# Kernel optimization log

Measured on AMD Instinct MI355X. Metric: run time of the kernel, lower is better.

## Reference

```python
import jax, jax.numpy as jnp
import numpy as np

B, L, DM = 2, 4096, 1024
DI = 2048      # expand * d_model
DT = 64        # dt_rank = ceil(d_model/16)
K = 4          # d_conv


def _silu(v):
    return v * jax.nn.sigmoid(v)


def setup_inputs() -> dict:
    key = jax.random.key(0)
    ks = jax.random.split(key, 9)
    s = lambda k, shape, sc: jax.random.normal(k, shape, dtype=jnp.float32) * sc
    return {
        "x": s(ks[0], (B, L, DM), 1.0),
        "in_proj_w": s(ks[1], (2 * DI, DM), 0.02),
        "conv_w": s(ks[2], (DI, 1, K), 0.1),   # depthwise: [out=DI, in/groups=1, k]
        "conv_b": s(ks[3], (DI,), 0.02),
        "x_proj_w": s(ks[4], (DT, DI), 0.02),
        "dt_proj_w": s(ks[5], (DI, DT), 0.02),
        "dt_proj_b": s(ks[6], (DI,), 0.02),
        "A_log": jax.random.uniform(ks[7], (DI,), jnp.float32, -3.0, -1.0),
        "D": jnp.ones((DI,), jnp.float32),
        "out_proj_w": s(ks[8], (DM, DI), 0.02),
    }


def reference(x, in_proj_w, conv_w, conv_b, x_proj_w, dt_proj_w, dt_proj_b,
              A_log, D, out_proj_w):
    b, l, _ = x.shape
    # input projection and gate split
    xz = jnp.einsum('bld,ed->ble', x, in_proj_w)          # [b,l,2*DI]
    xi, z = jnp.split(xz, 2, axis=-1)                     # each [b,l,DI]
    # depthwise causal conv1d (torch: padding=K-1 both sides, keep first L)
    xc = jnp.transpose(xi, (0, 2, 1))                     # [b,DI,l]
    xc = jax.lax.conv_general_dilated(
        xc, conv_w, window_strides=(1,), padding=[(K - 1, 0)],
        dimension_numbers=('NCH', 'OIH', 'NCH'),
        feature_group_count=xc.shape[1])
    xc = xc + conv_b[None, :, None]
    xi = _silu(jnp.transpose(xc, (0, 2, 1)))              # [b,l,DI]
    # dt path: x_proj -> dt_rank, dt_proj -> d_inner, softplus + clamp
    dt_low = jnp.einsum('bld,rd->blr', xi, x_proj_w)      # [b,l,DT]
    delta = jax.nn.softplus(jnp.einsum('blr,dr->bld', dt_low, dt_proj_w) + dt_proj_b)
    delta = jnp.clip(delta, 1e-6, 10.0)                   # [b,l,DI]
    A = jnp.clip(-jnp.exp(A_log), -10.0, -1e-6)           # [DI]
    e = jnp.clip(jnp.exp(delta * A), 1e-6, 1.0)           # decay factors [b,l,DI]

    # selective scan: state = clip(state*e + u)
    def step(state, eu):
        et, ut = eu
        state = jnp.clip(state * et + ut, -1e4, 1e4)
        return state, state

    init = jnp.zeros((b, xi.shape[-1]), xi.dtype)
    _, states = jax.lax.scan(step, init,
                             (jnp.swapaxes(e, 0, 1), jnp.swapaxes(xi, 0, 1)))
    y = jnp.swapaxes(states, 0, 1) + xi * D               # skip connection
    y = jnp.clip(y, -1e4, 1e4)
    y = y * _silu(z)                                      # gate
    return jnp.einsum('bld,ed->ble', y, out_proj_w)       # [b,l,DM]
```

## Files before the change

kernel.cpp:

```cpp
#include <hip/hip_runtime.h>
#include <cstdint>
#include <cstddef>

#define B_   2
#define L_   4096
#define DM_  1024
#define DI_  2048
#define DT_  64
#define M_   (B_*L_)
#define G_   64
#define CH_  (L_/G_)
#define KSPL 8
#define KSL  (DI_/KSPL)
#define BK_  32
#define LDC  136
#define LDCF 68
#define LDC3 132

typedef __bf16 bf16;
typedef __bf16 bf16x8 __attribute__((ext_vector_type(8)));
typedef __bf16 bf16x4 __attribute__((ext_vector_type(4)));
typedef float  f32x4  __attribute__((ext_vector_type(4)));

__device__ __forceinline__ float silu_f(float x){ return x / (1.f + __expf(-x)); }
__device__ __forceinline__ float softplus_f(float x){
  return fmaxf(x, 0.f) + __logf(1.f + __expf(-fabsf(x)));
}
__device__ __forceinline__ float e_of(float delta, float Ad){
  float ee = __expf(delta * Ad);
  return fminf(fmaxf(ee, 1e-6f), 1.f);
}
__device__ __forceinline__ float a_of(const float* alog, int d){
  float Ad = -__expf(alog[d]);
  return fminf(fmaxf(Ad, -10.f), -1e-6f);
}

__device__ __forceinline__ void gl_lds16(const bf16* g, bf16* l){
  __builtin_amdgcn_global_load_lds(
      (const __attribute__((address_space(1))) void*)g,
      (__attribute__((address_space(3))) void*)l, 16, 0, 0);
}

__global__ __launch_bounds__(256)
void cvt_all_kernel(const float4* __restrict__ s0, bf16x4* __restrict__ d0, int n0,
                    const float4* __restrict__ s1, bf16x4* __restrict__ d1, int n1,
                    const float4* __restrict__ s2, bf16x4* __restrict__ d2, int n2,
                    const float4* __restrict__ s3, bf16x4* __restrict__ d3, int n3,
                    const float4* __restrict__ s4, bf16x4* __restrict__ d4, int n4)
{
  int i = blockIdx.x*256 + threadIdx.x;
  const float4* s; bf16x4* d;
  if      (i < n0)                 { s = s0; d = d0; }
  else if ((i -= n0) < n1)         { s = s1; d = d1; }
  else if ((i -= n1) < n2)         { s = s2; d = d2; }
  else if ((i -= n2) < n3)         { s = s3; d = d3; }
  else if ((i -= n3) < n4)         { s = s4; d = d4; }
  else return;
  float4 v = s[i];
  bf16x4 o = {(bf16)v.x, (bf16)v.y, (bf16)v.z, (bf16)v.w};
  d[i] = o;
}

template<int EPI, int MT, int NT, int KT>
__global__ __launch_bounds__(256)
void gemm_bt(const bf16* __restrict__ A, const bf16* __restrict__ W,
             float* __restrict__ o0, bf16* __restrict__ ob, bf16* __restrict__ ob2,
             const float* __restrict__ bias, const float* __restrict__ alog,
             const bf16* __restrict__ uq, float* __restrict__ Pq,
             float* __restrict__ Fq)
{
  __shared__ char smem[34816];
  bf16* As = (bf16*)smem;
  bf16* Bs = (bf16*)(smem + 128*BK_*2);
  const int t    = threadIdx.x;
  const int lane = t & 63;
  const int wave = t >> 6;
  const int wm   = wave >> 1, wn = wave & 1;
  const int l16  = lane & 15, quad = lane >> 4;

  int m0, n0;
  if (EPI == 4){
    m0 = blockIdx.y * 128; n0 = 0;
  } else {
    const int gx  = NT / 128;
    const int lin = blockIdx.y * gx + blockIdx.x;
    const int grp = lin / (gx * 4);
    const int rem = lin % (gx * 4);
    m0 = (grp * 4 + (rem & 3)) * 128;
    n0 = (rem >> 2) * 128;
  }

  const int srow = (lane >> 2);
  const int scol = (lane & 3) * 8;

  const int KFULL = (EPI == 4) ? (KT * KSPL) : KT;
  const int kbase = (EPI == 4) ? (int)blockIdx.z * KT : 0;

  const int rowA0 = m0 + wave*32 + srow;
  int rB0 = n0 + wave*32 + srow, rB1 = rB0 + 16;
  if (NT < 128){ rB0 = (rB0 >= NT) ? NT-1 : rB0; rB1 = (rB1 >= NT) ? NT-1 : rB1; }
  const bf16* ap0 = A + (size_t)rowA0*KFULL        + kbase + scol;
  const bf16* ap1 = A + (size_t)(rowA0+16)*KFULL   + kbase + scol;
  const bf16* bp0 = W + (size_t)rB0*KFULL          + kbase + scol;
  const bf16* bp1 = W + (size_t)rB1*KFULL          + kbase + scol;
  bf16* lA0 = &As[(wave*32)*BK_];
  bf16* lA1 = &As[(wave*32+16)*BK_];
  bf16* lB0 = &Bs[(wave*32)*BK_];
  bf16* lB1 = &Bs[(wave*32+16)*BK_];

  f32x4 acc[4][4] = {};
  constexpr int kframes = KT / BK_;

  for (int kt = 0; kt < kframes; ++kt){
    gl_lds16(ap0, lA0);  gl_lds16(ap1, lA1);
    gl_lds16(bp0, lB0);  gl_lds16(bp1, lB1);
    ap0 += BK_; ap1 += BK_; bp0 += BK_; bp1 += BK_;
    __syncthreads();
    bf16x8 af[4], bf_[4];
    #pragma unroll
    for (int i = 0; i < 4; ++i){
      af[i]  = *(const bf16x8*)&As[(wm*64 + i*16 + l16)*BK_ + quad*8];
      bf_[i] = *(const bf16x8*)&Bs[(wn*64 + i*16 + l16)*BK_ + quad*8];
    }
    #pragma unroll
    for (int mi = 0; mi < 4; ++mi)
      #pragma unroll
      for (int ni = 0; ni < 4; ++ni)
        acc[mi][ni] = __builtin_amdgcn_mfma_f32_16x16x32_bf16(af[mi], bf_[ni], acc[mi][ni], 0, 0, 0);
    __syncthreads();
  }

  if (EPI == 3){
    float* Cf = (float*)smem;
    #pragma unroll
    for (int pass = 0; pass < 2; ++pass){
      if (wm == pass){
        #pragma unroll
        for (int mi = 0; mi < 4; ++mi)
          #pragma unroll
          for (int ni = 0; ni < 4; ++ni)
            #pragma unroll
            for (int r = 0; r < 4; ++r)
              Cf[(mi*16 + quad*4 + r)*LDC3 + wn*64 + ni*16 + l16] = acc[mi][ni][r];
      }
      __syncthreads();
      #pragma unroll
      for (int it = 0; it < 8; ++it){
        const int row = it*8 + (t >> 5);
        const int c4  = (t & 31) * 4;
        float4 v = *(const float4*)&Cf[row*LDC3 + c4];
        *(float4*)&o0[(size_t)(m0 + pass*64 + row)*NT + n0 + c4] = v;
      }
      __syncthreads();
    }
  } else if (EPI == 4){
    float* Cf = (float*)smem;
    if (wn == 0){
      #pragma unroll
      for (int mi = 0; mi < 4; ++mi)
        #pragma unroll
        for (int ni = 0; ni < 4; ++ni)
          #pragma unroll
          for (int r = 0; r < 4; ++r)
            Cf[(wm*64 + mi*16 + quad*4 + r)*LDCF + ni*16 + l16] = acc[mi][ni][r];
    }
    __syncthreads();
    #pragma unroll
    for (int it = 0; it < 8; ++it){
      const int row = it*16 + (t >> 4);
      const int c4  = (t & 15) * 4;
      float4 v = *(const float4*)&Cf[row*LDCF + c4];
      *(float4*)&o0[((size_t)blockIdx.z*M_ + m0 + row)*DT_ + c4] = v;
    }
  } else {
    bf16* Cs = (bf16*)smem;
    #pragma unroll
    for (int mi = 0; mi < 4; ++mi){
      #pragma unroll
      for (int ni = 0; ni < 4; ++ni){
        const int n = n0 + wn*64 + ni*16 + l16;
        #pragma unroll
        for (int r = 0; r < 4; ++r){
          float v = acc[mi][ni][r];
          if (EPI == 0){
            if (n0 >= DI_) v = silu_f(v);
          } else {
            v = softplus_f(v + bias[n]);
            v = fminf(fmaxf(v, 1e-6f), 10.f);
          }
          Cs[(wm*64 + mi*16 + quad*4 + r)*LDC + wn*64 + ni*16 + l16] = (bf16)v;
        }
      }
    }
    __syncthreads();
    #pragma unroll
    for (int it = 0; it < 8; ++it){
      const int row = it*16 + (t >> 4);
      const int c8  = (t & 15) * 8;
      bf16x8 v = *(const bf16x8*)&Cs[row*LDC + c8];
      if (EPI == 0){
        if (n0 < DI_) *(bf16x8*)&ob [(size_t)(m0+row)*DI_ + n0        + c8] = v;
        else          *(bf16x8*)&ob2[(size_t)(m0+row)*DI_ + n0 - DI_  + c8] = v;
      } else {
        *(bf16x8*)&ob[(size_t)(m0+row)*NT + n0 + c8] = v;
      }
    }
    if (EPI == 2){
      const int chunk = t >> 7;
      const int dcol  = t & 127;
      const int dglob = n0 + dcol;
      const float Ad  = a_of(alog, dglob);
      const int b  = m0 >> 12;
      const int c0 = (m0 & 4095) >> 6;
      const size_t ubase = (size_t)(m0 + chunk*64)*DI_ + dglob;
      float p = 1.f, f = 0.f;
      for (int i = 0; i < CH_; ++i){
        float dl = (float)Cs[(chunk*64 + i)*LDC + dcol];
        float ee = e_of(dl, Ad);
        float uu = (float)uq[ubase + (size_t)i*DI_];
        f = f*ee + uu;
        p *= ee;
      }
      const size_t o = ((size_t)(b*G_ + c0 + chunk))*DI_ + dglob;
      Pq[o] = p; Fq[o] = f;
    }
  }
}

__global__ __launch_bounds__(256)
void dt_reduce_kernel(const float* __restrict__ part, bf16* __restrict__ dtl){
  const int i = blockIdx.x*256 + threadIdx.x;
  float s = 0.f;
  #pragma unroll
  for (int z = 0; z < KSPL; ++z) s += part[(size_t)z*M_*DT_ + i];
  dtl[i] = (bf16)s;
}

__global__ __launch_bounds__(256)
void conv_silu_kernel(const bf16* __restrict__ xi, const float* __restrict__ cw,
                      const float* __restrict__ cb, bf16* __restrict__ ubf)
{
  const int idx = blockIdx.x*256 + threadIdx.x;
  const int d = idx & (DI_-1);
  const int l = (idx >> 11) & (L_-1);
  float s = cb[d];
  #pragma unroll
  for (int k = 0; k < 4; ++k){
    const int ll = l + k - 3;
    if (ll >= 0) s += (float)xi[idx + (k-3)*DI_] * cw[d*4 + k];
  }
  ubf[idx] = (bf16)silu_f(s);
}

__global__ __launch_bounds__(256)
void scan_pass3(const bf16* __restrict__ delta, const bf16* __restrict__ u,
                const bf16* __restrict__ g, const float* __restrict__ P,
                const float* __restrict__ F, const float* __restrict__ alog,
                const float* __restrict__ Dp, bf16* __restrict__ y)
{
  const int d = blockIdx.x*256 + threadIdx.x;
  const int c = blockIdx.y, b = blockIdx.z;
  const float Ad = a_of(alog, d);
  float s = 0.f;
  for (int cc = 0; cc < c; ++cc){
    const size_t o = ((size_t)(b*G_ + cc))*DI_ + d;
    s = F[o] + P[o]*s;
  }
  size_t base = ((size_t)(b*L_ + c*CH_))*DI_ + d;
  const float Dd = Dp[d];
  for (int i = 0; i < CH_; ++i){
    const size_t idx = base + (size_t)i*DI_;
    const float uu = (float)u[idx];
    s = s*e_of((float)delta[idx], Ad) + uu;
    float yy = s + uu*Dd;
    yy = fminf(fmaxf(yy, -1e4f), 1e4f);
    yy *= (float)g[idx];
    y[idx] = (bf16)yy;
  }
}

extern "C" void kernel_launch(void* const* d_in, const int* in_sizes, int n_in,
                              void* d_out, int out_size, void* d_ws, size_t ws_size,
                              hipStream_t stream)
{
  (void)in_sizes; (void)n_in; (void)out_size; (void)ws_size;
  const float* x        = (const float*)d_in[0];
  const float* in_w     = (const float*)d_in[1];
  const float* conv_w   = (const float*)d_in[2];
  const float* conv_b   = (const float*)d_in[3];
  const float* xproj_w  = (const float*)d_in[4];
  const float* dtproj_w = (const float*)d_in[5];
  const float* dtproj_b = (const float*)d_in[6];
  const float* A_log    = (const float*)d_in[7];
  const float* Dp       = (const float*)d_in[8];
  const float* out_w    = (const float*)d_in[9];

  char* base = (char*)d_ws;
  const size_t MiB = 1024*1024;
  bf16*  xi_bf = (bf16*) (base + 0);
  float* part  = (float*)(base + 0);
  bf16*  dl_bf = (bf16*) (base + 0);
  bf16*  x_bf  = (bf16*) (base + 32*MiB);
  bf16*  w1_bf = (bf16*) (base + 48*MiB);
  bf16*  g_bf  = (bf16*) (base + 64*MiB);
  bf16*  u_bf  = (bf16*) (base + 96*MiB);
  bf16*  y_bf  = (bf16*) (base + 128*MiB);
  bf16*  wo_bf = (bf16*) (base + 160*MiB);
  bf16*  xp_bf = (bf16*) (base + 164*MiB);
  bf16*  dp_bf = (bf16*) (base + 165*MiB);
  bf16*  dtl_bf= (bf16*) (base + 166*MiB);
  float* P     = (float*)(base + 167*MiB);
  float* F     = (float*)(base + 168*MiB);

  const int c0 = (M_*DM_)/4, c1 = (2*DI_*DM_)/4, c2 = (DT_*DI_)/4,
            c3 = (DI_*DT_)/4, c4 = (DM_*DI_)/4;
  const int ctot = c0+c1+c2+c3+c4;
  cvt_all_kernel<<<(ctot+255)/256, 256, 0, stream>>>(
      (const float4*)x,        (bf16x4*)x_bf,  c0,
      (const float4*)in_w,     (bf16x4*)w1_bf, c1,
      (const float4*)xproj_w,  (bf16x4*)xp_bf, c2,
      (const float4*)dtproj_w, (bf16x4*)dp_bf, c3,
      (const float4*)out_w,    (bf16x4*)wo_bf, c4);

  gemm_bt<0, M_, 2*DI_, DM_><<<dim3((2*DI_)/128, M_/128), 256, 0, stream>>>(
      x_bf, w1_bf, nullptr, xi_bf, g_bf, nullptr,
      nullptr, nullptr, nullptr, nullptr);
  conv_silu_kernel<<<(M_*DI_)/256, 256, 0, stream>>>(xi_bf, conv_w, conv_b, u_bf);
  gemm_bt<4, M_, DT_, KSL><<<dim3(1, M_/128, KSPL), 256, 0, stream>>>(
      u_bf, xp_bf, part, nullptr, nullptr, nullptr,
      nullptr, nullptr, nullptr, nullptr);
  dt_reduce_kernel<<<(M_*DT_)/256, 256, 0, stream>>>(part, dtl_bf);
  gemm_bt<2, M_, DI_, DT_><<<dim3(DI_/128, M_/128), 256, 0, stream>>>(
      dtl_bf, dp_bf, nullptr, dl_bf, nullptr, dtproj_b,
      A_log, u_bf, P, F);
  scan_pass3<<<dim3(DI_/256, G_, B_), 256, 0, stream>>>(
      dl_bf, u_bf, g_bf, P, F, A_log, Dp, y_bf);
  gemm_bt<3, M_, DM_, DI_><<<dim3(DM_/128, M_/128), 256, 0, stream>>>(
      y_bf, wo_bf, (float*)d_out, nullptr, nullptr, nullptr,
      nullptr, nullptr, nullptr, nullptr);
}
```

Before: 419.7 us.

## Replace in_proj GEMM with 256x256-tile double-buffered direct-to-LDS kernel

Adds a dedicated gemm256 kernel for the input projection. It uses 512 threads and 256x256 output tiles, loads global memory directly into swizzled LDS with double buffering, and remaps blocks so that groups of them share tiles. Wave priority is raised around the MFMA bursts. The aim is more data reuse per tile and better overlap of loads with compute than the generic 128x128 gemm_bt. The cost is 128KB of LDS per block, which limits occupancy, and a more complex epilogue that writes the output in two passes.

After: 405.2 us. 3.5% less time.

```diff
diff --git a/kernel.cpp b/kernel.cpp
--- a/kernel.cpp
+++ b/kernel.cpp
@@ -61,6 +61,135 @@
   d[i] = o;
 }
 
+template<int MT, int NT, int KT>
+__global__ __launch_bounds__(512, 2)
+void gemm256(const bf16* __restrict__ A, const bf16* __restrict__ W,
+             bf16* __restrict__ ob, bf16* __restrict__ ob2)
+{
+  __shared__ __align__(16) char smem[131072];
+  char* lA = smem;
+  char* lB = smem + 65536;
+
+  const int t    = threadIdx.x;
+  const int lane = t & 63;
+  const int wave = t >> 6;
+  const int wm   = wave >> 2;
+  const int wn   = wave & 3;
+  const int l16  = lane & 15, quad = lane >> 4;
+
+  const int nnt = NT / 256;
+  const int nwg = (MT/256) * nnt;
+  const int cpx = nwg >> 3;
+  int lin = (blockIdx.x & 7) * cpx + (blockIdx.x >> 3);
+  const int m0 = (lin / nnt) * 256;
+  const int n0 = (lin % nnt) * 256;
+
+  const int r8     = lane >> 3;
+  const int lchunk = (lane & 7) ^ r8;
+  const bf16* ap[4]; const bf16* bp[4];
+  #pragma unroll
+  for (int s = 0; s < 4; ++s){
+    ap[s] = A + (size_t)(m0 + s*64 + wave*8 + r8) * KT + lchunk*8;
+    bp[s] = W + (size_t)(n0 + s*64 + wave*8 + r8) * KT + lchunk*8;
+  }
+
+  auto stage = [&](int ub){
+    #pragma unroll
+    for (int s = 0; s < 4; ++s){
+      gl_lds16(ap[s], (bf16*)(lA + ub*32768 + s*8192 + wave*1024));
+      ap[s] += 64;
+    }
+    #pragma unroll
+    for (int s = 0; s < 4; ++s){
+      gl_lds16(bp[s], (bf16*)(lB + ub*32768 + s*8192 + wave*1024));
+      bp[s] += 64;
+    }
+  };
+
+  f32x4 acc[8][4] = {};
+  constexpr int NTILES = KT / 64;
+
+  stage(0);
+  for (int tt = 0; tt < NTILES; ++tt){
+    const int u = tt & 1;
+    if (tt + 1 < NTILES){
+      stage(u ^ 1);
+      asm volatile("s_waitcnt vmcnt(8)" ::: "memory");
+    } else {
+      asm volatile("s_waitcnt vmcnt(0)" ::: "memory");
+    }
+    __builtin_amdgcn_s_barrier();
+    __builtin_amdgcn_sched_barrier(0);
+    const char* Ab = lA + u*32768;
+    const char* Bb = lB + u*32768;
+
+    #pragma unroll
+    for (int ph = 0; ph < 4; ++ph){
+      const int qm = ph >> 1, qn = ph & 1;
+      bf16x8 af[2][4], bfr[2][2];
+      #pragma unroll
+      for (int s = 0; s < 2; ++s)
+        #pragma unroll
+        for (int mi = 0; mi < 4; ++mi){
+          const int row = wm*128 + qm*64 + mi*16 + l16;
+          af[s][mi] = *(const bf16x8*)(Ab + row*128 +
+                        ((((s<<2)|quad) ^ (l16 & 7)) << 4));
+        }
+      #pragma unroll
+      for (int s = 0; s < 2; ++s)
+        #pragma unroll
+        for (int ni = 0; ni < 2; ++ni){
+          const int row = wn*64 + qn*32 + ni*16 + l16;
+          bfr[s][ni] = *(const bf16x8*)(Bb + row*128 +
+                        ((((s<<2)|quad) ^ (l16 & 7)) << 4));
+        }
+      asm volatile("s_waitcnt lgkmcnt(0)" ::: "memory");
+      __builtin_amdgcn_sched_barrier(0);
+      __builtin_amdgcn_s_setprio(1);
+      #pragma unroll
+      for (int s = 0; s < 2; ++s)
+        #pragma unroll
+        for (int mi = 0; mi < 4; ++mi)
+          #pragma unroll
+          for (int ni = 0; ni < 2; ++ni)
+            acc[qm*4+mi][qn*2+ni] = __builtin_amdgcn_mfma_f32_16x16x32_bf16(
+                af[s][mi], bfr[s][ni], acc[qm*4+mi][qn*2+ni], 0, 0, 0);
+      __builtin_amdgcn_s_setprio(0);
+      __builtin_amdgcn_sched_barrier(0);
+    }
+    __builtin_amdgcn_s_barrier();
+  }
+
+  bf16* Cs = (bf16*)smem;
+  const bool isg  = (n0 >= DI_);
+  bf16* outp      = isg ? ob2 : ob;
+  const int ncol0 = isg ? (n0 - DI_) : n0;
+  #pragma unroll
+  for (int pass = 0; pass < 2; ++pass){
+    if (wm == pass){
+      #pragma unroll
+      for (int mi = 0; mi < 8; ++mi)
+        #pragma unroll
+        for (int ni = 0; ni < 4; ++ni)
+          #pragma unroll
+          for (int r = 0; r < 4; ++r){
+            float v = acc[mi][ni][r];
+            if (isg) v = silu_f(v);
+            Cs[(mi*16 + quad*4 + r)*264 + wn*64 + ni*16 + l16] = (bf16)v;
+          }
+    }
+    __syncthreads();
+    #pragma unroll
+    for (int it = 0; it < 8; ++it){
+      const int row = it*16 + (t >> 5);
+      const int c8  = (t & 31) * 8;
+      bf16x8 v = *(const bf16x8*)&Cs[row*264 + c8];
+      *(bf16x8*)&outp[(size_t)(m0 + pass*128 + row)*DI_ + ncol0 + c8] = v;
+    }
+    __syncthreads();
+  }
+}
+
 template<int EPI, int MT, int NT, int KT>
 __global__ __launch_bounds__(256)
 void gemm_bt(const bf16* __restrict__ A, const bf16* __restrict__ W,
@@ -182,12 +311,8 @@
         #pragma unroll
         for (int r = 0; r < 4; ++r){
           float v = acc[mi][ni][r];
-          if (EPI == 0){
-            if (n0 >= DI_) v = silu_f(v);
-          } else {
-            v = softplus_f(v + bias[n]);
-            v = fminf(fmaxf(v, 1e-6f), 10.f);
-          }
+          v = softplus_f(v + bias[n]);
+          v = fminf(fmaxf(v, 1e-6f), 10.f);
           Cs[(wm*64 + mi*16 + quad*4 + r)*LDC + wn*64 + ni*16 + l16] = (bf16)v;
         }
       }
@@ -198,14 +323,9 @@
       const int row = it*16 + (t >> 4);
       const int c8  = (t & 15) * 8;
       bf16x8 v = *(const bf16x8*)&Cs[row*LDC + c8];
-      if (EPI == 0){
-        if (n0 < DI_) *(bf16x8*)&ob [(size_t)(m0+row)*DI_ + n0        + c8] = v;
-        else          *(bf16x8*)&ob2[(size_t)(m0+row)*DI_ + n0 - DI_  + c8] = v;
-      } else {
-        *(bf16x8*)&ob[(size_t)(m0+row)*NT + n0 + c8] = v;
-      }
-    }
-    if (EPI == 2){
+      *(bf16x8*)&ob[(size_t)(m0+row)*NT + n0 + c8] = v;
+    }
+    {
       const int chunk = t >> 7;
       const int dcol  = t & 127;
       const int dglob = n0 + dcol;
@@ -322,9 +442,8 @@
       (const float4*)dtproj_w, (bf16x4*)dp_bf, c3,
       (const float4*)out_w,    (bf16x4*)wo_bf, c4);
 
-  gemm_bt<0, M_, 2*DI_, DM_><<<dim3((2*DI_)/128, M_/128), 256, 0, stream>>>(
-      x_bf, w1_bf, nullptr, xi_bf, g_bf, nullptr,
-      nullptr, nullptr, nullptr, nullptr);
+  gemm256<M_, 2*DI_, DM_><<<dim3((M_/256)*((2*DI_)/256)), 512, 0, stream>>>(
+      x_bf, w1_bf, xi_bf, g_bf);
   conv_silu_kernel<<<(M_*DI_)/256, 256, 0, stream>>>(xi_bf, conv_w, conv_b, u_bf);
   gemm_bt<4, M_, DT_, KSL><<<dim3(1, M_/128, KSPL), 256, 0, stream>>>(
       u_bf, xp_bf, part, nullptr, nullptr, nullptr,
```
